# Kernel tuning notes

Measured on AMD Instinct MI355X. Metric: run time of the kernel, lower is better.

## Reference

```python
import jax, jax.numpy as jnp
import numpy as np

SCALE = 0.08838834764831845  # head_dim ** -0.5
NUM_HEADS = 32
NUM_KV_HEADS = 8
HEAD_DIM = 128
PAGE_SIZE = 16


def setup_inputs() -> dict:
    key = jax.random.key(0)
    k1, k2 = jax.random.split(key)
    B = 32
    L0_PAGES = 256        # shared prefix: 4096 tokens
    L1_PAGES = 64         # per-seq chunk: 1024 tokens
    L2_PAGES = 32         # per-seq suffix: 512 tokens
    P = L0_PAGES + B * L1_PAGES + B * L2_PAGES  # 3328 pages
    q = jax.random.normal(k1, (B, NUM_HEADS * HEAD_DIM), jnp.float32)
    # paged KV cache, layout [page, k/v, page_size, kv_heads, head_dim]
    kv_cache = jax.random.normal(k2, (P, 2, PAGE_SIZE, NUM_KV_HEADS, HEAD_DIM), jnp.float32)
    shared_page_idx = jnp.arange(L0_PAGES, dtype=jnp.int32)
    seq1_page_idx = (L0_PAGES + jnp.arange(B * L1_PAGES, dtype=jnp.int32)).reshape(B, L1_PAGES)
    seq2_page_idx = (L0_PAGES + B * L1_PAGES + jnp.arange(B * L2_PAGES, dtype=jnp.int32)).reshape(B, L2_PAGES)
    return {"q": q, "kv_cache": kv_cache, "shared_page_idx": shared_page_idx,
            "seq1_page_idx": seq1_page_idx, "seq2_page_idx": seq2_page_idx}


def _softmax_attn(scores, V, av_eq):
    # scores: [..., L]; returns (out, lse) with a single stable pass
    m = scores.max(axis=-1, keepdims=True)
    e = jnp.exp(scores - m)
    denom = e.sum(axis=-1)
    out = jnp.einsum(av_eq, e, V) / denom[..., None]
    lse = m[..., 0] + jnp.log(denom)
    return out, lse


def _merge_state(oa, sa, ob, sb):
    # flashinfer.merge_state: LSE-weighted combination of attention states
    s = jnp.logaddexp(sa, sb)
    o = oa * jnp.exp(sa - s)[..., None] + ob * jnp.exp(sb - s)[..., None]
    return o, s


def _forward(q, kv_cache, shared_page_idx, seq1_page_idx, seq2_page_idx):
    B = q.shape[0]
    G = NUM_HEADS // NUM_KV_HEADS  # GQA group size = 4
    # q -> [B, Hkv, G, D]
    q4 = q.reshape(B, NUM_KV_HEADS, G, HEAD_DIM)

    # level 0: shared pages -> [L0, Hkv, D]
    K0 = kv_cache[shared_page_idx, 0].reshape(-1, NUM_KV_HEADS, HEAD_DIM)
    V0 = kv_cache[shared_page_idx, 1].reshape(-1, NUM_KV_HEADS, HEAD_DIM)
    s0 = jnp.einsum('bkgd,lkd->bkgl', q4, K0) * SCALE
    out, lse = _softmax_attn(s0, V0, 'bkgl,lkd->bkgd')

    # levels 1 and 2: per-sequence paged KV -> [B, Li, Hkv, D]
    for idx in (seq1_page_idx, seq2_page_idx):
        Ki = kv_cache[idx, 0].reshape(B, -1, NUM_KV_HEADS, HEAD_DIM)
        Vi = kv_cache[idx, 1].reshape(B, -1, NUM_KV_HEADS, HEAD_DIM)
        si = jnp.einsum('bkgd,blkd->bkgl', q4, Ki) * SCALE
        oi, li = _softmax_attn(si, Vi, 'bkgl,blkd->bkgd')
        out, lse = _merge_state(out, lse, oi, li)

    return out.reshape(B, NUM_HEADS * HEAD_DIM)


def reference(q, kv_cache, shared_page_idx, seq1_page_idx, seq2_page_idx):
    return _forward(q, kv_cache, shared_page_idx, seq1_page_idx, seq2_page_idx)
```

## Files before the change

### kernel.cpp

```cpp
#include <hip/hip_runtime.h>
#include <stdint.h>


namespace {
constexpr int kG = 4, kD = 128;
constexpr float kQS = 0.08838834764831845f * 1.4426950408889634f;
constexpr int kNChunk = 64;
constexpr int kNSplit = 3;
constexpr int kNSrc = kNChunk + kNSplit;
constexpr size_t kOParts = (size_t)kNSrc * 32 * 8 * 4 * 128;
constexpr size_t kMLB = kOParts;
constexpr size_t kWsFloats = kOParts + (size_t)kNSrc * 32 * 8 * 4 * 2;
}

__device__ __forceinline__ float wave_max(float v) {
#pragma unroll
    for (int off = 1; off < 64; off <<= 1) v = fmaxf(v, __shfl_xor(v, off));
    return v;
}
__device__ __forceinline__ float wave_sum(float v) {
#pragma unroll
    for (int off = 1; off < 64; off <<= 1) v += __shfl_xor(v, off);
    return v;
}
__device__ __forceinline__ int kslot(int s, int t) { return s ^ (t & 31); }
__device__ __forceinline__ int vslot(int s, int t) {
    return s ^ (((t << 1) & 31) | ((t >> 4) & 1));
}

__global__ __launch_bounds__(512, 2)
void fused_kernel(const float* __restrict__ q, const float* __restrict__ kv,
                  const int* __restrict__ sp0, const int* __restrict__ sp1,
                  const int* __restrict__ sp2, float* __restrict__ ws)
{
    __shared__ __align__(16) float smem[16384];
    __shared__ int pgs[4];

    const int bid = blockIdx.x;
    const int grp = bid / 5, rem = bid % 5;
    const int tid = threadIdx.x;
    const int w = tid >> 6, lane = tid & 63;
    const int ts = lane >> 4, dg = lane & 15;

    if (rem < 2) {
        const int lid = grp * 2 + rem;
        const int h = lid & 7, c4 = lid >> 3;
        if (tid < 4) pgs[tid] = sp0[c4 * 4 + tid];
        __syncthreads();
        {
            const int t = tid >> 3;
            const int sg = (tid & 7) * 4;
            const int pg = pgs[t >> 4];
            const float* gk = kv + (size_t)pg * 32768u + (size_t)(t & 15) * 1024u + h * 128;
#pragma unroll
            for (int j = 0; j < 4; ++j) {
                const int s = sg + j;
                *(float4*)&smem[t * 128 + (kslot(s, t) << 2)] =
                    *(const float4*)(gk + s * 4);
                *(float4*)&smem[8192 + t * 128 + (vslot(s, t) << 2)] =
                    *(const float4*)(gk + 16384 + s * 4);
            }
        }
        __syncthreads();

        const int wq = __builtin_amdgcn_readfirstlane(w);
        for (int pass = 0; pass < 4; ++pass) {
            const int b = wq * 4 + pass;
            const float* qb = q + (size_t)b * 4096 + h * 512;
            float s[4] = {0.f, 0.f, 0.f, 0.f};
#pragma unroll
            for (int c = 0; c < 16; ++c) {
                float4 ka = *(const float4*)&smem[lane * 128 + (kslot(2 * c, lane) << 2)];
                float4 kb = *(const float4*)&smem[lane * 128 + (kslot(2 * c + 1, lane) << 2)];
#pragma unroll
                for (int g = 0; g < 4; ++g) {
                    float4 qa = *(const float4*)(qb + g * 128 + c * 8);
                    float4 q2 = *(const float4*)(qb + g * 128 + c * 8 + 4);
                    s[g] += ka.x * qa.x + ka.y * qa.y + ka.z * qa.z + ka.w * qa.w
                          + kb.x * q2.x + kb.y * q2.y + kb.z * q2.z + kb.w * q2.w;
                }
            }
            float m[4], p[4], l[4], acc[4][8];
#pragma unroll
            for (int g = 0; g < 4; ++g) {
                s[g] *= kQS;
                m[g] = wave_max(s[g]);
                p[g] = exp2f(s[g] - m[g]);
                l[g] = wave_sum(p[g]);
#pragma unroll
                for (int e = 0; e < 8; ++e) acc[g][e] = 0.f;
            }
#pragma unroll
            for (int j = 0; j < 16; ++j) {
                const int t = ts * 16 + j;
                float4 va = *(const float4*)&smem[8192 + t * 128 + (vslot(2 * dg, t) << 2)];
                float4 vb = *(const float4*)&smem[8192 + t * 128 + (vslot(2 * dg + 1, t) << 2)];
#pragma unroll
                for (int g = 0; g < 4; ++g) {
                    float pj = __shfl(p[g], t);
                    acc[g][0] = fmaf(pj, va.x, acc[g][0]);
                    acc[g][1] = fmaf(pj, va.y, acc[g][1]);
                    acc[g][2] = fmaf(pj, va.z, acc[g][2]);
                    acc[g][3] = fmaf(pj, va.w, acc[g][3]);
                    acc[g][4] = fmaf(pj, vb.x, acc[g][4]);
                    acc[g][5] = fmaf(pj, vb.y, acc[g][5]);
                    acc[g][6] = fmaf(pj, vb.z, acc[g][6]);
                    acc[g][7] = fmaf(pj, vb.w, acc[g][7]);
                }
            }
#pragma unroll
            for (int g = 0; g < 4; ++g)
#pragma unroll
                for (int e = 0; e < 8; ++e) {
                    float v = acc[g][e];
                    v += __shfl_xor(v, 16);
                    v += __shfl_xor(v, 32);
                    acc[g][e] = v;
                }
            if (lane < 16) {
                const size_t ob = ((((size_t)c4 * 32 + b) * 8 + h) * 4) * 128 + lane * 8;
#pragma unroll
                for (int g = 0; g < 4; ++g) {
                    *(float4*)&ws[ob + (size_t)g * 128] =
                        make_float4(acc[g][0], acc[g][1], acc[g][2], acc[g][3]);
                    *(float4*)&ws[ob + (size_t)g * 128 + 4] =
                        make_float4(acc[g][4], acc[g][5], acc[g][6], acc[g][7]);
                }
            }
            if (lane == 0) {
                const size_t idx = (((size_t)c4 * 32 + b) * 8 + h) * 4;
#pragma unroll
                for (int g = 0; g < 4; ++g) {
                    ws[kMLB + 2 * (idx + g)] = m[g];
                    ws[kMLB + 2 * (idx + g) + 1] = l[g];
                }
            }
        }
    } else {
        const int sid = grp * 3 + (rem - 2);
        const int split = sid >> 8;
        const int b = (sid & 255) >> 3;
        const int h = sid & 7;
        float* wacc = smem;
        float* wm = smem + 4096;
        float* wl = smem + 4128;
        int* plist = (int*)(smem + 4160);

        if (tid < 32) {
            const int gi = split * 32 + tid;
            plist[tid] = (gi < 64) ? sp1[b * 64 + gi] : sp2[b * 32 + (gi - 64)];
        }
        __syncthreads();

        const int page = plist[w * 4 + ts];
        const size_t poff = (size_t)page * 32768u;
        const float* Kp = kv + poff + (size_t)(lane & 15) * 1024u + h * 128;
        const float* Vp = kv + poff + 16384u + h * 128 + dg * 8;
        const float* qb = q + (size_t)b * 4096 + h * 512;

        float s[kG] = {0.f, 0.f, 0.f, 0.f};
#pragma unroll
        for (int c = 0; c < 16; ++c) {
            float4 ka = *(const float4*)(Kp + c * 8);
            float4 kb = *(const float4*)(Kp + c * 8 + 4);
#pragma unroll
            for (int g = 0; g < kG; ++g) {
                float4 qa = *(const float4*)(qb + g * 128 + c * 8);
                float4 q2 = *(const float4*)(qb + g * 128 + c * 8 + 4);
                s[g] += ka.x * qa.x + ka.y * qa.y + ka.z * qa.z + ka.w * qa.w
                      + kb.x * q2.x + kb.y * q2.y + kb.z * q2.z + kb.w * q2.w;
            }
        }
        float m[kG], p[kG], l[kG], acc[kG][8];
#pragma unroll
        for (int g = 0; g < kG; ++g) {
            s[g] *= kQS;
            m[g] = wave_max(s[g]);
            p[g] = exp2f(s[g] - m[g]);
            l[g] = wave_sum(p[g]);
#pragma unroll
            for (int e = 0; e < 8; ++e) acc[g][e] = 0.f;
        }
#pragma unroll
        for (int j = 0; j < 16; ++j) {
            const int t = ts * 16 + j;
            float4 va = *(const float4*)(Vp + (size_t)j * 1024u);
            float4 vb = *(const float4*)(Vp + (size_t)j * 1024u + 4);
#pragma unroll
            for (int g = 0; g < kG; ++g) {
                float pj = __shfl(p[g], t);
                acc[g][0] = fmaf(pj, va.x, acc[g][0]);
                acc[g][1] = fmaf(pj, va.y, acc[g][1]);
                acc[g][2] = fmaf(pj, va.z, acc[g][2]);
                acc[g][3] = fmaf(pj, va.w, acc[g][3]);
                acc[g][4] = fmaf(pj, vb.x, acc[g][4]);
                acc[g][5] = fmaf(pj, vb.y, acc[g][5]);
                acc[g][6] = fmaf(pj, vb.z, acc[g][6]);
                acc[g][7] = fmaf(pj, vb.w, acc[g][7]);
            }
        }
#pragma unroll
        for (int g = 0; g < kG; ++g)
#pragma unroll
            for (int e = 0; e < 8; ++e) {
                float v = acc[g][e];
                v += __shfl_xor(v, 16);
                v += __shfl_xor(v, 32);
                acc[g][e] = v;
            }
        if (lane < 16) {
#pragma unroll
            for (int g = 0; g < kG; ++g) {
                *(float4*)&wacc[w * 512 + g * 128 + dg * 8] =
                    make_float4(acc[g][0], acc[g][1], acc[g][2], acc[g][3]);
                *(float4*)&wacc[w * 512 + g * 128 + dg * 8 + 4] =
                    make_float4(acc[g][4], acc[g][5], acc[g][6], acc[g][7]);
            }
            if (lane == 0)
#pragma unroll
                for (int g = 0; g < kG; ++g) { wm[w * 4 + g] = m[g]; wl[w * 4 + g] = l[g]; }
        }
        __syncthreads();

        {
            const int g = tid >> 7, d = tid & 127;
            float mstar = wm[g];
#pragma unroll
            for (int ww = 1; ww < 8; ++ww) mstar = fmaxf(mstar, wm[ww * 4 + g]);
            float numer = 0.f, denom = 0.f;
#pragma unroll
            for (int ww = 0; ww < 8; ++ww) {
                float sc = exp2f(wm[ww * 4 + g] - mstar);
                denom = fmaf(sc, wl[ww * 4 + g], denom);
                numer = fmaf(sc, wacc[ww * 512 + g * 128 + d], numer);
            }
            const size_t src = (size_t)(kNChunk + split);
            const size_t ob = (((src * 32 + b) * 8 + h) * 4 + g) * 128 + d;
            ws[ob] = numer;
            if (d == 0) {
                const size_t idx = ((src * 32 + b) * 8 + h) * 4 + g;
                ws[kMLB + 2 * idx] = mstar;
                ws[kMLB + 2 * idx + 1] = denom;
            }
        }
    }
}

__global__ __launch_bounds__(512, 4)
void merge_kernel(const float* __restrict__ ws, float* __restrict__ out)
{
    __shared__ float sm[kNSrc][4], sl[kNSrc][4];
    const int b = blockIdx.x >> 3, h = blockIdx.x & 7;
    const int tid = threadIdx.x;
    if (tid < kNSrc * 4) {
        const int src = tid >> 2, g = tid & 3;
        const size_t idx = ((((size_t)src * 32 + b) * 8 + h) * 4 + g);
        sm[src][g] = ws[kMLB + 2 * idx];
        sl[src][g] = ws[kMLB + 2 * idx + 1];
    }
    __syncthreads();
    const int g = tid >> 7, d = tid & 127;
    float mstar = -1e30f;
#pragma unroll
    for (int s = 0; s < kNSrc; ++s) mstar = fmaxf(mstar, sm[s][g]);
    float numer = 0.f, denom = 0.f;
#pragma unroll 4
    for (int s = 0; s < kNSrc; ++s) {
        const float sc = exp2f(sm[s][g] - mstar);
        denom = fmaf(sc, sl[s][g], denom);
        const size_t ob = ((((size_t)s * 32 + b) * 8 + h) * 4 + g) * 128 + d;
        numer = fmaf(sc, ws[ob], numer);
    }
    out[(size_t)b * 4096 + h * 512 + g * 128 + d] = numer / denom;
}

__global__ __launch_bounds__(512, 2)
void fallback_kernel(const float* __restrict__ q, const float* __restrict__ kv,
                     const int* __restrict__ sp0, const int* __restrict__ sp1,
                     const int* __restrict__ sp2, float* __restrict__ out)
{
    __shared__ __align__(16) float qs[kG * kD];
    __shared__ int plist[352];
    __shared__ __align__(16) float wacc[8][kG * kD];
    __shared__ float wm[8][kG], wl[8][kG];
    const int b = blockIdx.x >> 3, h = blockIdx.x & 7;
    const int tid = threadIdx.x;
    {
        const int g = tid >> 7, d = tid & 127;
        qs[g * 128 + d] = q[(size_t)b * 4096 + h * 512 + g * 128 + d] * kQS;
    }
    if (tid < 352) {
        int pg;
        if (tid < 256)      pg = sp0[tid];
        else if (tid < 320) pg = sp1[b * 64 + (tid - 256)];
        else                pg = sp2[b * 32 + (tid - 320)];
        plist[tid] = pg;
    }
    __syncthreads();
    const int w = tid >> 6, lane = tid & 63;
    const int ts = lane >> 4, dg = lane & 15;
    const float4* qv4 = (const float4*)qs;
    float m[kG], l[kG], acc[kG][8];
#pragma unroll
    for (int g = 0; g < kG; ++g) {
        m[g] = -1e30f; l[g] = 0.f;
#pragma unroll
        for (int e = 0; e < 8; ++e) acc[g][e] = 0.f;
    }
    for (int tile = 0; tile < 11; ++tile) {
        const int page = plist[w * 44 + tile * 4 + ts];
        const size_t poff = (size_t)page * 32768u;
        const float* Kp = kv + poff + (size_t)(lane & 15) * 1024u + h * 128;
        const float* Vp = kv + poff + 16384u + h * 128 + dg * 8;
        float s[kG] = {0.f, 0.f, 0.f, 0.f};
#pragma unroll
        for (int c = 0; c < 16; ++c) {
            float4 ka = *(const float4*)(Kp + c * 8);
            float4 kb = *(const float4*)(Kp + c * 8 + 4);
#pragma unroll
            for (int g = 0; g < kG; ++g) {
                float4 qa = qv4[g * 32 + c * 2];
                float4 qb = qv4[g * 32 + c * 2 + 1];
                s[g] += ka.x * qa.x + ka.y * qa.y + ka.z * qa.z + ka.w * qa.w
                      + kb.x * qb.x + kb.y * qb.y + kb.z * qb.z + kb.w * qb.w;
            }
        }
        float p[kG];
#pragma unroll
        for (int g = 0; g < kG; ++g) {
            float mt = wave_max(s[g]);
            float mn = fmaxf(m[g], mt);
            float alpha = exp2f(m[g] - mn);
            p[g] = exp2f(s[g] - mn);
            m[g] = mn;
            l[g] = l[g] * alpha + wave_sum(p[g]);
#pragma unroll
            for (int e = 0; e < 8; ++e) acc[g][e] *= alpha;
        }
#pragma unroll
        for (int j = 0; j < 16; ++j) {
            const int t = ts * 16 + j;
            float4 va = *(const float4*)(Vp + (size_t)j * 1024u);
            float4 vb = *(const float4*)(Vp + (size_t)j * 1024u + 4);
#pragma unroll
            for (int g = 0; g < kG; ++g) {
                float pj = __shfl(p[g], t);
                acc[g][0] = fmaf(pj, va.x, acc[g][0]);
                acc[g][1] = fmaf(pj, va.y, acc[g][1]);
                acc[g][2] = fmaf(pj, va.z, acc[g][2]);
                acc[g][3] = fmaf(pj, va.w, acc[g][3]);
                acc[g][4] = fmaf(pj, vb.x, acc[g][4]);
                acc[g][5] = fmaf(pj, vb.y, acc[g][5]);
                acc[g][6] = fmaf(pj, vb.z, acc[g][6]);
                acc[g][7] = fmaf(pj, vb.w, acc[g][7]);
            }
        }
    }
#pragma unroll
    for (int g = 0; g < kG; ++g)
#pragma unroll
        for (int e = 0; e < 8; ++e) {
            float v = acc[g][e];
            v += __shfl_xor(v, 16);
            v += __shfl_xor(v, 32);
            acc[g][e] = v;
        }
    if (lane < 16) {
#pragma unroll
        for (int g = 0; g < kG; ++g) {
            *(float4*)&wacc[w][g * 128 + dg * 8]     = make_float4(acc[g][0], acc[g][1], acc[g][2], acc[g][3]);
            *(float4*)&wacc[w][g * 128 + dg * 8 + 4] = make_float4(acc[g][4], acc[g][5], acc[g][6], acc[g][7]);
        }
        if (lane == 0)
#pragma unroll
            for (int g = 0; g < kG; ++g) { wm[w][g] = m[g]; wl[w][g] = l[g]; }
    }
    __syncthreads();
    {
        const int g = tid >> 7, d = tid & 127;
        float mstar = wm[0][g];
#pragma unroll
        for (int ww = 1; ww < 8; ++ww) mstar = fmaxf(mstar, wm[ww][g]);
        float numer = 0.f, denom = 0.f;
#pragma unroll
        for (int ww = 0; ww < 8; ++ww) {
            float sc = exp2f(wm[ww][g] - mstar);
            denom = fmaf(sc, wl[ww][g], denom);
            numer = fmaf(sc, wacc[ww][g * 128 + d], numer);
        }
        out[(size_t)b * 4096 + h * 512 + g * 128 + d] = numer / denom;
    }
}

extern "C" void kernel_launch(void* const* d_in, const int* in_sizes, int n_in,
                              void* d_out, int out_size, void* d_ws, size_t ws_size,
                              hipStream_t stream) {
    const float* q  = (const float*)d_in[0];
    const float* kv = (const float*)d_in[1];
    const int* sp0 = (const int*)d_in[2];
    const int* sp1 = (const int*)d_in[3];
    const int* sp2 = (const int*)d_in[4];
    float* out = (float*)d_out;
    float* ws = (float*)d_ws;
    if (ws_size >= kWsFloats * sizeof(float)) {
        hipLaunchKernelGGL(fused_kernel, dim3(1280), dim3(512), 0, stream,
                           q, kv, sp0, sp1, sp2, ws);
        hipLaunchKernelGGL(merge_kernel, dim3(256), dim3(512), 0, stream, ws, out);
    } else {
        hipLaunchKernelGGL(fallback_kernel, dim3(256), dim3(512), 0, stream,
                           q, kv, sp0, sp1, sp2, out);
    }
}
```

Measured before the change: 730.4 us.

## Split per-sequence attention into fine page tiles with direct-to-LDS loads

Per-sequence levels are now divided into 24 tiles of 4 pages per (batch, head), giving 6144 small blocks interleaved with the level-0 blocks instead of 3 large splits. Each tile stages K/V into swizzled LDS with global_load_lds, and four waves each handle one query in the group, writing partial states straight to the workspace. This removes the in-block cross-wave merge. The merge kernel is restructured to one block per (b,h,g) with batched loads, trading more parallelism for more partial states and more merge traffic. Half the waves in each tile block only load and do no compute.

```diff
diff --git a/kernel.cpp b/kernel.cpp
--- a/kernel.cpp
+++ b/kernel.cpp
@@ -6,8 +6,8 @@
 constexpr int kG = 4, kD = 128;
 constexpr float kQS = 0.08838834764831845f * 1.4426950408889634f;
 constexpr int kNChunk = 64;
-constexpr int kNSplit = 3;
-constexpr int kNSrc = kNChunk + kNSplit;
+constexpr int kNTile = 24;
+constexpr int kNSrc = kNChunk + kNTile;
 constexpr size_t kOParts = (size_t)kNSrc * 32 * 8 * 4 * 128;
 constexpr size_t kMLB = kOParts;
 constexpr size_t kWsFloats = kOParts + (size_t)kNSrc * 32 * 8 * 4 * 2;
@@ -26,6 +26,11 @@
 __device__ __forceinline__ int kslot(int s, int t) { return s ^ (t & 31); }
 __device__ __forceinline__ int vslot(int s, int t) {
     return s ^ (((t << 1) & 31) | ((t >> 4) & 1));
+}
+__device__ __forceinline__ void gll16(const float* gp, float* lp) {
+    __builtin_amdgcn_global_load_lds(
+        (const __attribute__((address_space(1))) void*)gp,
+        (__attribute__((address_space(3))) void*)lp, 16, 0, 0);
 }
 
 __global__ __launch_bounds__(512, 2)
@@ -37,14 +42,13 @@
     __shared__ int pgs[4];
 
     const int bid = blockIdx.x;
-    const int grp = bid / 5, rem = bid % 5;
     const int tid = threadIdx.x;
     const int w = tid >> 6, lane = tid & 63;
     const int ts = lane >> 4, dg = lane & 15;
-
-    if (rem < 2) {
-        const int lid = grp * 2 + rem;
-        const int h = lid & 7, c4 = lid >> 3;
+    const int l0id = bid / 13;
+
+    if (bid % 13 == 0) {
+        const int h = l0id & 7, c4 = l0id >> 3;
         if (tid < 4) pgs[tid] = sp0[c4 * 4 + tid];
         __syncthreads();
         {
@@ -137,141 +141,123 @@
             }
         }
     } else {
-        const int sid = grp * 3 + (rem - 2);
-        const int split = sid >> 8;
-        const int b = (sid & 255) >> 3;
-        const int h = sid & 7;
-        float* wacc = smem;
-        float* wm = smem + 4096;
-        float* wl = smem + 4128;
-        int* plist = (int*)(smem + 4160);
-
-        if (tid < 32) {
-            const int gi = split * 32 + tid;
-            plist[tid] = (gi < 64) ? sp1[b * 64 + gi] : sp2[b * 32 + (gi - 64)];
+        const int sid = bid - l0id - 1;
+        const int b = sid / 192;
+        const int h = (sid / 24) & 7;
+        const int tle = sid % 24;
+        const int wq = __builtin_amdgcn_readfirstlane(w);
+
+        const int jw = tle * 4 + (wq >> 1);
+        const int pgw = (jw < 64) ? sp1[b * 64 + jw] : sp2[b * 32 + (jw - 64)];
+        const size_t poff = (size_t)pgw * 32768u;
+
+        {
+            const int sl = lane & 31;
+            const int rl = lane >> 5;
+#pragma unroll
+            for (int i = 0; i < 4; ++i) {
+                const int r = wq * 8 + i * 2 + rl;
+                const float* gk = kv + poff + (size_t)(r & 15) * 1024u + h * 128;
+                gll16(gk + ((sl ^ (r & 31)) << 2),
+                      &smem[wq * 1024 + i * 256]);
+                const int vm = ((r << 1) & 31) | ((r >> 4) & 1);
+                gll16(gk + 16384 + ((sl ^ vm) << 2),
+                      &smem[8192 + wq * 1024 + i * 256]);
+            }
         }
         __syncthreads();
 
-        const int page = plist[w * 4 + ts];
-        const size_t poff = (size_t)page * 32768u;
-        const float* Kp = kv + poff + (size_t)(lane & 15) * 1024u + h * 128;
-        const float* Vp = kv + poff + 16384u + h * 128 + dg * 8;
-        const float* qb = q + (size_t)b * 4096 + h * 512;
-
-        float s[kG] = {0.f, 0.f, 0.f, 0.f};
-#pragma unroll
-        for (int c = 0; c < 16; ++c) {
-            float4 ka = *(const float4*)(Kp + c * 8);
-            float4 kb = *(const float4*)(Kp + c * 8 + 4);
-#pragma unroll
-            for (int g = 0; g < kG; ++g) {
-                float4 qa = *(const float4*)(qb + g * 128 + c * 8);
-                float4 q2 = *(const float4*)(qb + g * 128 + c * 8 + 4);
-                s[g] += ka.x * qa.x + ka.y * qa.y + ka.z * qa.z + ka.w * qa.w
-                      + kb.x * q2.x + kb.y * q2.y + kb.z * q2.z + kb.w * q2.w;
-            }
-        }
-        float m[kG], p[kG], l[kG], acc[kG][8];
-#pragma unroll
-        for (int g = 0; g < kG; ++g) {
-            s[g] *= kQS;
-            m[g] = wave_max(s[g]);
-            p[g] = exp2f(s[g] - m[g]);
-            l[g] = wave_sum(p[g]);
-#pragma unroll
-            for (int e = 0; e < 8; ++e) acc[g][e] = 0.f;
-        }
-#pragma unroll
-        for (int j = 0; j < 16; ++j) {
-            const int t = ts * 16 + j;
-            float4 va = *(const float4*)(Vp + (size_t)j * 1024u);
-            float4 vb = *(const float4*)(Vp + (size_t)j * 1024u + 4);
-#pragma unroll
-            for (int g = 0; g < kG; ++g) {
-                float pj = __shfl(p[g], t);
-                acc[g][0] = fmaf(pj, va.x, acc[g][0]);
-                acc[g][1] = fmaf(pj, va.y, acc[g][1]);
-                acc[g][2] = fmaf(pj, va.z, acc[g][2]);
-                acc[g][3] = fmaf(pj, va.w, acc[g][3]);
-                acc[g][4] = fmaf(pj, vb.x, acc[g][4]);
-                acc[g][5] = fmaf(pj, vb.y, acc[g][5]);
-                acc[g][6] = fmaf(pj, vb.z, acc[g][6]);
-                acc[g][7] = fmaf(pj, vb.w, acc[g][7]);
-            }
-        }
-#pragma unroll
-        for (int g = 0; g < kG; ++g)
+        if (wq < 4) {
+            const int g = wq;
+            const float* qb = q + (size_t)b * 4096 + h * 512 + g * 128;
+            float s = 0.f;
+#pragma unroll
+            for (int c = 0; c < 16; ++c) {
+                float4 ka = *(const float4*)&smem[lane * 128 + (kslot(2 * c, lane) << 2)];
+                float4 kb = *(const float4*)&smem[lane * 128 + (kslot(2 * c + 1, lane) << 2)];
+                float4 qa = *(const float4*)(qb + c * 8);
+                float4 q2 = *(const float4*)(qb + c * 8 + 4);
+                s += ka.x * qa.x + ka.y * qa.y + ka.z * qa.z + ka.w * qa.w
+                   + kb.x * q2.x + kb.y * q2.y + kb.z * q2.z + kb.w * q2.w;
+            }
+            s *= kQS;
+            const float m = wave_max(s);
+            const float p = exp2f(s - m);
+            const float l = wave_sum(p);
+            float acc[8];
+#pragma unroll
+            for (int e = 0; e < 8; ++e) acc[e] = 0.f;
+#pragma unroll
+            for (int j = 0; j < 16; ++j) {
+                const int t = ts * 16 + j;
+                float4 va = *(const float4*)&smem[8192 + t * 128 + (vslot(2 * dg, t) << 2)];
+                float4 vb = *(const float4*)&smem[8192 + t * 128 + (vslot(2 * dg + 1, t) << 2)];
+                const float pj = __shfl(p, t);
+                acc[0] = fmaf(pj, va.x, acc[0]);
+                acc[1] = fmaf(pj, va.y, acc[1]);
+                acc[2] = fmaf(pj, va.z, acc[2]);
+                acc[3] = fmaf(pj, va.w, acc[3]);
+                acc[4] = fmaf(pj, vb.x, acc[4]);
+                acc[5] = fmaf(pj, vb.y, acc[5]);
+                acc[6] = fmaf(pj, vb.z, acc[6]);
+                acc[7] = fmaf(pj, vb.w, acc[7]);
+            }
 #pragma unroll
             for (int e = 0; e < 8; ++e) {
-                float v = acc[g][e];
+                float v = acc[e];
                 v += __shfl_xor(v, 16);
                 v += __shfl_xor(v, 32);
-                acc[g][e] = v;
-            }
-        if (lane < 16) {
-#pragma unroll
-            for (int g = 0; g < kG; ++g) {
-                *(float4*)&wacc[w * 512 + g * 128 + dg * 8] =
-                    make_float4(acc[g][0], acc[g][1], acc[g][2], acc[g][3]);
-                *(float4*)&wacc[w * 512 + g * 128 + dg * 8 + 4] =
-                    make_float4(acc[g][4], acc[g][5], acc[g][6], acc[g][7]);
-            }
-            if (lane == 0)
-#pragma unroll
-                for (int g = 0; g < kG; ++g) { wm[w * 4 + g] = m[g]; wl[w * 4 + g] = l[g]; }
-        }
-        __syncthreads();
-
-        {
-            const int g = tid >> 7, d = tid & 127;
-            float mstar = wm[g];
-#pragma unroll
-            for (int ww = 1; ww < 8; ++ww) mstar = fmaxf(mstar, wm[ww * 4 + g]);
-            float numer = 0.f, denom = 0.f;
-#pragma unroll
-            for (int ww = 0; ww < 8; ++ww) {
-                float sc = exp2f(wm[ww * 4 + g] - mstar);
-                denom = fmaf(sc, wl[ww * 4 + g], denom);
-                numer = fmaf(sc, wacc[ww * 512 + g * 128 + d], numer);
-            }
-            const size_t src = (size_t)(kNChunk + split);
-            const size_t ob = (((src * 32 + b) * 8 + h) * 4 + g) * 128 + d;
-            ws[ob] = numer;
-            if (d == 0) {
+                acc[e] = v;
+            }
+            const size_t src = (size_t)(kNChunk + tle);
+            if (lane < 16) {
+                const size_t ob = (((src * 32 + b) * 8 + h) * 4 + g) * 128 + lane * 8;
+                *(float4*)&ws[ob]     = make_float4(acc[0], acc[1], acc[2], acc[3]);
+                *(float4*)&ws[ob + 4] = make_float4(acc[4], acc[5], acc[6], acc[7]);
+            }
+            if (lane == 0) {
                 const size_t idx = ((src * 32 + b) * 8 + h) * 4 + g;
-                ws[kMLB + 2 * idx] = mstar;
-                ws[kMLB + 2 * idx + 1] = denom;
-            }
-        }
-    }
-}
-
-__global__ __launch_bounds__(512, 4)
+                ws[kMLB + 2 * idx] = m;
+                ws[kMLB + 2 * idx + 1] = l;
+            }
+        }
+    }
+}
+
+__global__ __launch_bounds__(128, 8)
 void merge_kernel(const float* __restrict__ ws, float* __restrict__ out)
 {
-    __shared__ float sm[kNSrc][4], sl[kNSrc][4];
-    const int b = blockIdx.x >> 3, h = blockIdx.x & 7;
+    __shared__ float sm[kNSrc], sls[kNSrc], sc[kNSrc];
+    const int bid = blockIdx.x;
+    const int b = bid >> 5, h = (bid >> 2) & 7, g = bid & 3;
     const int tid = threadIdx.x;
-    if (tid < kNSrc * 4) {
-        const int src = tid >> 2, g = tid & 3;
-        const size_t idx = ((((size_t)src * 32 + b) * 8 + h) * 4 + g);
-        sm[src][g] = ws[kMLB + 2 * idx];
-        sl[src][g] = ws[kMLB + 2 * idx + 1];
+    if (tid < kNSrc) {
+        const size_t idx = (((size_t)tid * 32 + b) * 8 + h) * 4 + g;
+        sm[tid]  = ws[kMLB + 2 * idx];
+        sls[tid] = ws[kMLB + 2 * idx + 1];
     }
     __syncthreads();
-    const int g = tid >> 7, d = tid & 127;
     float mstar = -1e30f;
 #pragma unroll
-    for (int s = 0; s < kNSrc; ++s) mstar = fmaxf(mstar, sm[s][g]);
-    float numer = 0.f, denom = 0.f;
-#pragma unroll 4
-    for (int s = 0; s < kNSrc; ++s) {
-        const float sc = exp2f(sm[s][g] - mstar);
-        denom = fmaf(sc, sl[s][g], denom);
-        const size_t ob = ((((size_t)s * 32 + b) * 8 + h) * 4 + g) * 128 + d;
-        numer = fmaf(sc, ws[ob], numer);
-    }
-    out[(size_t)b * 4096 + h * 512 + g * 128 + d] = numer / denom;
+    for (int s = 0; s < kNSrc; ++s) mstar = fmaxf(mstar, sm[s]);
+    if (tid < kNSrc) sc[tid] = exp2f(sm[tid] - mstar);
+    __syncthreads();
+    float denom = 0.f;
+#pragma unroll
+    for (int s = 0; s < kNSrc; ++s) denom = fmaf(sc[s], sls[s], denom);
+    const size_t base = ((((size_t)b * 8 + h) * 4 + g) * 128) + tid;
+    float numer = 0.f;
+#pragma unroll 1
+    for (int s0 = 0; s0 < kNSrc; s0 += 8) {
+        float v[8];
+#pragma unroll
+        for (int k = 0; k < 8; ++k)
+            v[k] = ws[base + (size_t)(s0 + k) * 131072u];
+#pragma unroll
+        for (int k = 0; k < 8; ++k)
+            numer = fmaf(sc[s0 + k], v[k], numer);
+    }
+    out[(size_t)b * 4096 + h * 512 + g * 128 + tid] = numer / denom;
 }
 
 __global__ __launch_bounds__(512, 2)
@@ -403,9 +389,9 @@
     float* out = (float*)d_out;
     float* ws = (float*)d_ws;
     if (ws_size >= kWsFloats * sizeof(float)) {
-        hipLaunchKernelGGL(fused_kernel, dim3(1280), dim3(512), 0, stream,
+        hipLaunchKernelGGL(fused_kernel, dim3(6656), dim3(512), 0, stream,
                            q, kv, sp0, sp1, sp2, ws);
-        hipLaunchKernelGGL(merge_kernel, dim3(256), dim3(512), 0, stream, ws, out);
+        hipLaunchKernelGGL(merge_kernel, dim3(1024), dim3(128), 0, stream, ws, out);
     } else {
         hipLaunchKernelGGL(fallback_kernel, dim3(256), dim3(512), 0, stream,
                            q, kv, sp0, sp1, sp2, out);
```

New measurement: 819.0 us. +12.1%, slower.
